# Optimization experiments

Hardware: AMD Instinct MI355X
Metric: run time of the kernel (lower is better)

The kernel has to match this reference:

```python
import jax, jax.numpy as jnp
import numpy as np

N, K, D, VOCAB = 20000, 32, 128, 100000
NEG = -1e30  # finite large-negative so all-masked rows don't produce NaN softmax


def setup_inputs() -> dict:
    key = jax.random.key(0)
    ks = jax.random.split(key, 10)
    return {
        "nodes": jax.random.randint(ks[0], (N,), 0, VOCAB),
        "neigh_idx": jax.random.randint(ks[1], (N, K), 0, VOCAB),
        "neigh_len": jax.random.randint(ks[2], (N,), 0, K + 1),
        "u2e": jax.random.normal(ks[3], (VOCAB, D), dtype=jnp.float32),
        "W1": jax.random.normal(ks[4], (D, 2 * D), dtype=jnp.float32) * 0.05,
        "b1": jax.random.normal(ks[5], (D,), dtype=jnp.float32) * 0.05,
        "W2": jax.random.normal(ks[6], (D, D), dtype=jnp.float32) * 0.05,
        "b2": jax.random.normal(ks[7], (D,), dtype=jnp.float32) * 0.05,
        "W3": jax.random.normal(ks[8], (1, D), dtype=jnp.float32) * 0.05,
        "b3": jax.random.normal(ks[9], (1,), dtype=jnp.float32) * 0.05,
    }


def reference(nodes, neigh_idx, neigh_len, u2e, W1, b1, W2, b2, W3, b3):
    # self features: [N, D]
    self_feats = u2e[nodes]
    # neighbor features gather: [N, K, D]
    e_u = u2e[neigh_idx]
    # GraphRec Attention: cat(neighbor, self-broadcast) -> MLP -> softmax over K
    x = jnp.concatenate(
        [e_u, jnp.broadcast_to(self_feats[:, None, :], e_u.shape)], axis=-1
    )  # [N, K, 2D]
    h = jax.nn.relu(jnp.einsum("nkf,df->nkd", x, W1) + b1)
    h = jax.nn.relu(jnp.einsum("nkd,ed->nke", h, W2) + b2)
    logits = jnp.einsum("nkd,od->nko", h, W3)[..., 0] + b3[0]  # [N, K]
    mask = jnp.arange(K)[None, :] < neigh_len[:, None]  # [N, K]
    att = jax.nn.softmax(jnp.where(mask, logits, NEG), axis=1)
    att = jnp.where(mask, att, 0.0)  # zero out padded slots (and all-empty rows)
    # attention-weighted neighbor aggregation: [N, D]
    agg = jnp.einsum("nk,nkd->nd", att, e_u)
    has_neigh = (neigh_len > 0)[:, None]
    return jnp.where(has_neigh, (agg + self_feats) * 0.5, self_feats)
```

## Files before the change

kernel.cpp:

```cpp
#include <hip/hip_runtime.h>
#include <hip/hip_bf16.h>
#include <stdint.h>

#define KN 32
#define D  128
#define NNODES 20000
#define GRID 2500
#define ITERS 4
#define VOCAB 100000
#define CONV_BLOCKS (VOCAB * D / 2048)

typedef __bf16 bf16;
typedef __bf16 bf16x8 __attribute__((ext_vector_type(8)));
typedef float  f32x4  __attribute__((ext_vector_type(4)));

#define CHUNK_E 520
#define EU_NODE_E (8 * CHUNK_E)
#define H_STRIDE 136

#define GL2LDS(src, dst) __builtin_amdgcn_global_load_lds(                 \
    (const __attribute__((address_space(1))) void*)(src),                  \
    (__attribute__((address_space(3))) void*)(dst), 16, 0, 0)

#define MFMA(a, b, c) __builtin_amdgcn_mfma_f32_16x16x32_bf16((a), (b), (c), 0, 0, 0)

#define LBAR() do {                                                        \
    asm volatile("s_waitcnt lgkmcnt(0)" ::: "memory");                     \
    __builtin_amdgcn_s_barrier();                                          \
    asm volatile("" ::: "memory");                                         \
    __builtin_amdgcn_sched_barrier(0);                                     \
} while (0)

__global__ __launch_bounds__(256) void pack_weights_kernel(
    const float* __restrict__ W1, const float* __restrict__ W2,
    bf16* __restrict__ w1p, bf16* __restrict__ w2p)
{
    int t = blockIdx.x * 256 + threadIdx.x;
    if (t < 32768) {
        int j = t & 7, lane = (t >> 3) & 63, kt = (t >> 9) & 7, nt = t >> 12;
        int d = nt * 16 + (lane & 15);
        int f = kt * 32 + ((lane >> 4) << 3) + j;
        w1p[t] = (bf16)W1[d * 256 + f];
    } else if (t < 49152) {
        int u = t - 32768;
        int j = u & 7, lane = (u >> 3) & 63, kt = (u >> 9) & 3, nt = u >> 11;
        int e  = nt * 16 + (lane & 15);
        int dd = kt * 32 + ((lane >> 4) << 3) + j;
        w2p[u] = (bf16)W2[e * 128 + dd];
    }
}

__global__ __launch_bounds__(256) void prep_kernel(
    const float* __restrict__ u2e, const float* __restrict__ W1,
    const float* __restrict__ W2,
    bf16* __restrict__ tbl, bf16* __restrict__ w1p, bf16* __restrict__ w2p)
{
    int b = blockIdx.x;
    if (b < CONV_BLOCKS) {
        size_t i = ((size_t)b * 256 + threadIdx.x) * 8;
        float4 a = *(const float4*)(u2e + i);
        float4 c = *(const float4*)(u2e + i + 4);
        bf16x8 v;
        v[0]=(bf16)a.x; v[1]=(bf16)a.y; v[2]=(bf16)a.z; v[3]=(bf16)a.w;
        v[4]=(bf16)c.x; v[5]=(bf16)c.y; v[6]=(bf16)c.z; v[7]=(bf16)c.w;
        *(bf16x8*)(tbl + i) = v;
    } else {
        int t = (b - CONV_BLOCKS) * 256 + threadIdx.x;
        if (t < 32768) {
            int j = t & 7, lane = (t >> 3) & 63, kt = (t >> 9) & 7, nt = t >> 12;
            int d = nt * 16 + (lane & 15);
            int f = kt * 32 + ((lane >> 4) << 3) + j;
            w1p[t] = (bf16)W1[d * 256 + f];
        } else if (t < 49152) {
            int u = t - 32768;
            int j = u & 7, lane = (u >> 3) & 63, kt = (u >> 9) & 3, nt = u >> 11;
            int e  = nt * 16 + (lane & 15);
            int dd = kt * 32 + ((lane >> 4) << 3) + j;
            w2p[u] = (bf16)W2[e * 128 + dd];
        }
    }
}

__global__ __launch_bounds__(256, 3) void graphrec_agg_kernel(
    const int*   __restrict__ nodes,
    const int*   __restrict__ neigh_idx,
    const int*   __restrict__ neigh_len,
    const float* __restrict__ u2e,
    const bf16*  __restrict__ u2e_bf,
    const float* __restrict__ b1,
    const float* __restrict__ b2,
    const float* __restrict__ W3,
    const float* __restrict__ b3,
    const bf16*  __restrict__ w1p,
    const bf16*  __restrict__ w2p,
    float*       __restrict__ out)
{
    __shared__ alignas(16) bf16  eu[2][2 * EU_NODE_E];
    __shared__ alignas(16) float self_f[2][2 * D];
    __shared__ alignas(16) bf16  h1[2 * KN * H_STRIDE];
    __shared__ float lpart[2][4 * KN];

    const int t    = threadIdx.x;
    const int lane = t & 63;
    const int wave = t >> 6;
    const int ln15 = lane & 15;
    const int quad = lane >> 4;
    const int nt0  = wave * 2;

    const float bias1_0 = b1[nt0 * 16 + ln15];
    const float bias1_1 = b1[(nt0 + 1) * 16 + ln15];
    const float bias2_0 = b2[nt0 * 16 + ln15];
    const float bias2_1 = b2[(nt0 + 1) * 16 + ln15];
    const float w3_0    = W3[nt0 * 16 + ln15];
    const float w3_1    = W3[(nt0 + 1) * 16 + ln15];
    const float b3v     = b3[0];

    bf16x8 w1e[2][4], w1s[2][4], w2r[2][4];
    #pragma unroll
    for (int nt = 0; nt < 2; ++nt) {
        #pragma unroll
        for (int ft = 0; ft < 4; ++ft) {
            w1e[nt][ft] = *(const bf16x8*)(w1p + ((nt0 + nt) * 8 + ft) * 512 + lane * 8);
            w1s[nt][ft] = *(const bf16x8*)(w1p + ((nt0 + nt) * 8 + 4 + ft) * 512 + lane * 8);
        }
        #pragma unroll
        for (int kt = 0; kt < 4; ++kt)
            w2r[nt][kt] = *(const bf16x8*)(w2p + ((nt0 + nt) * 4 + kt) * 512 + lane * 8);
    }

    auto STAGE = [&](int jt) {
        const int buf = jt & 1;
        const int nA2 = blockIdx.x * 8 + jt * 2;
        const int gnd = wave >> 1;
        const int cb  = (wave & 1) * 4;
        const int sA  = nodes[nA2];
        const int sB  = nodes[nA2 + 1];
        int4 idx4 = *(const int4*)(neigh_idx + (size_t)(nA2 + gnd) * KN + cb + (quad << 3));
        bf16* dst = &eu[buf][gnd * EU_NODE_E + cb * CHUNK_E];
        const size_t col = (size_t)(ln15 << 3);
        GL2LDS(u2e_bf + (size_t)idx4.x * D + col, dst);
        GL2LDS(u2e_bf + (size_t)idx4.y * D + col, dst + CHUNK_E);
        GL2LDS(u2e_bf + (size_t)idx4.z * D + col, dst + 2 * CHUNK_E);
        GL2LDS(u2e_bf + (size_t)idx4.w * D + col, dst + 3 * CHUNK_E);
        if (wave == 0) {
            int sidx = (lane >> 5) ? sB : sA;
            GL2LDS(u2e + (size_t)sidx * D + ((lane & 31) << 2), &self_f[buf][0]);
        }
    };

    STAGE(0);

    #pragma unroll 1
    for (int it = 0; it < ITERS; ++it) {
        const int nA   = blockIdx.x * 8 + it * 2;
        const int lenA = neigh_len[nA];
        const int lenB = neigh_len[nA + 1];

        if (it + 1 < ITERS) STAGE(it + 1);
        __builtin_amdgcn_sched_barrier(0);
        if (it == 0 || it + 1 == ITERS) {
            asm volatile("s_waitcnt vmcnt(0)" ::: "memory");
        } else if (wave == 0) {
            asm volatile("s_waitcnt vmcnt(6)" ::: "memory");
        } else {
            asm volatile("s_waitcnt vmcnt(5)" ::: "memory");
        }
        __builtin_amdgcn_s_barrier();
        asm volatile("" ::: "memory");
        __builtin_amdgcn_sched_barrier(0);

        const bf16*  euIt = &eu[it & 1][0];
        const float* sfIt = &self_f[it & 1][0];

        f32x4 cs0 = {0.f,0.f,0.f,0.f}, cs1 = cs0;
        {
            const float* sp = sfIt + (ln15 < 2 ? ln15 : 1) * D;
            #pragma unroll
            for (int kt = 0; kt < 4; ++kt) {
                f32x4 u0 = *(const f32x4*)(sp + kt * 32 + quad * 8);
                f32x4 u1 = *(const f32x4*)(sp + kt * 32 + quad * 8 + 4);
                bf16x8 a;
                #pragma unroll
                for (int e = 0; e < 4; ++e) { a[e] = (bf16)u0[e]; a[4 + e] = (bf16)u1[e]; }
                cs0 = MFMA(a, w1s[0][kt], cs0);
                cs1 = MFMA(a, w1s[1][kt], cs1);
            }
        }
        const float svA0 = __shfl(cs0[0], ln15);
        const float svB0 = __shfl(cs0[1], ln15);
        const float svA1 = __shfl(cs1[0], ln15);
        const float svB1 = __shfl(cs1[1], ln15);

        #pragma unroll 1
        for (int nd = 0; nd < 2; ++nd) {
            const bf16* euN = euIt + nd * EU_NODE_E;
            bf16* h1N = h1 + nd * KN * H_STRIDE;

            f32x4 c00 = {0.f,0.f,0.f,0.f}, c01 = c00, c10 = c00, c11 = c00;
            const int rb = (ln15 & 7) * CHUNK_E + (ln15 >> 3) * 128;
            #pragma unroll
            for (int ft = 0; ft < 4; ++ft) {
                bf16x8 a0 = *(const bf16x8*)(euN + rb + ft * 32 + quad * 8);
                bf16x8 a1 = *(const bf16x8*)(euN + rb + 256 + ft * 32 + quad * 8);
                c00 = MFMA(a0, w1e[0][ft], c00);
                c01 = MFMA(a0, w1e[1][ft], c01);
                c10 = MFMA(a1, w1e[0][ft], c10);
                c11 = MFMA(a1, w1e[1][ft], c11);
            }
            const float s0 = nd ? svB0 : svA0;
            const float s1 = nd ? svB1 : svA1;
            #pragma unroll
            for (int r = 0; r < 4; ++r) {
                int row = quad * 4 + r;
                h1N[row * H_STRIDE + nt0 * 16 + ln15]              = (bf16)fmaxf(c00[r] + bias1_0 + s0, 0.f);
                h1N[row * H_STRIDE + (nt0 + 1) * 16 + ln15]        = (bf16)fmaxf(c01[r] + bias1_1 + s1, 0.f);
                h1N[(16 + row) * H_STRIDE + nt0 * 16 + ln15]       = (bf16)fmaxf(c10[r] + bias1_0 + s0, 0.f);
                h1N[(16 + row) * H_STRIDE + (nt0 + 1) * 16 + ln15] = (bf16)fmaxf(c11[r] + bias1_1 + s1, 0.f);
            }
        }
        LBAR();

        #pragma unroll 1
        for (int nd = 0; nd < 2; ++nd) {
            const bf16* h1N = h1 + nd * KN * H_STRIDE;
            f32x4 d00 = {0.f,0.f,0.f,0.f}, d01 = d00, d10 = d00, d11 = d00;
            #pragma unroll
            for (int kt = 0; kt < 4; ++kt) {
                bf16x8 a0 = *(const bf16x8*)(h1N + ln15 * H_STRIDE + kt * 32 + quad * 8);
                bf16x8 a1 = *(const bf16x8*)(h1N + (16 + ln15) * H_STRIDE + kt * 32 + quad * 8);
                d00 = MFMA(a0, w2r[0][kt], d00);
                d01 = MFMA(a0, w2r[1][kt], d01);
                d10 = MFMA(a1, w2r[0][kt], d10);
                d11 = MFMA(a1, w2r[1][kt], d11);
            }
            #pragma unroll
            for (int r = 0; r < 4; ++r) {
                float p0 = w3_0 * fmaxf(d00[r] + bias2_0, 0.f)
                         + w3_1 * fmaxf(d01[r] + bias2_1, 0.f);
                float p1 = w3_0 * fmaxf(d10[r] + bias2_0, 0.f)
                         + w3_1 * fmaxf(d11[r] + bias2_1, 0.f);
                #pragma unroll
                for (int o = 1; o < 16; o <<= 1) {
                    p0 += __shfl_xor(p0, o);
                    p1 += __shfl_xor(p1, o);
                }
                if (ln15 == 0) {
                    lpart[nd][wave * KN + quad * 4 + r]      = p0;
                    lpart[nd][wave * KN + 16 + quad * 4 + r] = p1;
                }
            }
        }
        LBAR();

        {
            const int nd = wave >> 1;
            const int k  = lane & 31;
            float lg = lpart[nd][k] + lpart[nd][KN + k] + lpart[nd][2 * KN + k]
                     + lpart[nd][3 * KN + k] + b3v;
            const int len = nd ? lenB : lenA;
            bool act = k < len;
            float l = act ? lg : -1e30f;
            float m = l;
            #pragma unroll
            for (int o = 1; o < 32; o <<= 1) m = fmaxf(m, __shfl_xor(m, o));
            float e = act ? expf(l - m) : 0.f;
            float s = e;
            #pragma unroll
            for (int o = 1; o < 32; o <<= 1) s += __shfl_xor(s, o);
            float att = (s > 0.f) ? (e / s) : 0.f;

            const int d = ((wave & 1) << 6) + lane;
            const bf16* euN = euIt + nd * EU_NODE_E;
            float acc = 0.f;
            #pragma unroll
            for (int k2 = 0; k2 < KN; ++k2) {
                float a  = __shfl(att, k2);
                float ev = (float)euN[(k2 & 7) * CHUNK_E + (k2 >> 3) * 128 + (d & 127)];
                acc += a * ev;
            }
            float sf = sfIt[nd * D + (d & 127)];
            out[(size_t)(nA + nd) * D + (d & 127)] = (len > 0) ? 0.5f * (acc + sf) : sf;
        }
        LBAR();
    }
}

#define FB_CHUNK_DW 260
#define FB_EU_NODE_DW (16 * FB_CHUNK_DW)

__global__ __launch_bounds__(256, 3) void graphrec_agg_fb(
    const int*   __restrict__ nodes,
    const int*   __restrict__ neigh_idx,
    const int*   __restrict__ neigh_len,
    const float* __restrict__ u2e,
    const float* __restrict__ b1,
    const float* __restrict__ b2,
    const float* __restrict__ W3,
    const float* __restrict__ b3,
    const bf16*  __restrict__ w1p,
    const bf16*  __restrict__ w2p,
    float*       __restrict__ out)
{
    __shared__ alignas(16) float eu[2 * FB_EU_NODE_DW];
    __shared__ alignas(16) bf16  h1[2 * KN * H_STRIDE];
    __shared__ alignas(16) float self_f[2 * D];
    __shared__ float lpart[2][4 * KN];
    __shared__ float att_s[2][KN];

    const int t    = threadIdx.x;
    const int lane = t & 63;
    const int wave = t >> 6;
    const int ln15 = lane & 15;
    const int quad = lane >> 4;
    const int nt0  = wave * 2;

    const float bias1_0 = b1[nt0 * 16 + ln15];
    const float bias1_1 = b1[(nt0 + 1) * 16 + ln15];
    const float bias2_0 = b2[nt0 * 16 + ln15];
    const float bias2_1 = b2[(nt0 + 1) * 16 + ln15];
    const float w3_0    = W3[nt0 * 16 + ln15];
    const float w3_1    = W3[(nt0 + 1) * 16 + ln15];
    const float b3v     = b3[0];

    bf16x8 w1r[2][8];
    #pragma unroll
    for (int nt = 0; nt < 2; ++nt)
        #pragma unroll
        for (int ft = 0; ft < 8; ++ft)
            w1r[nt][ft] = *(const bf16x8*)(w1p + ((nt0 + nt) * 8 + ft) * 512 + lane * 8);
    bf16x8 w2r[2][4];
    #pragma unroll
    for (int nt = 0; nt < 2; ++nt)
        #pragma unroll
        for (int kt = 0; kt < 4; ++kt)
            w2r[nt][kt] = *(const bf16x8*)(w2p + ((nt0 + nt) * 4 + kt) * 512 + lane * 8);

    #pragma unroll 1
    for (int it = 0; it < ITERS; ++it) {
        const int nA   = blockIdx.x * 8 + it * 2;
        const int lenA = neigh_len[nA];
        const int lenB = neigh_len[nA + 1];
        {
            const int half = lane >> 5;
            const int colb = (lane & 31) << 4;
            #pragma unroll
            for (int nd = 0; nd < 2; ++nd) {
                #pragma unroll
                for (int j = 0; j < 4; ++j) {
                    int chunk = wave * 4 + j;
                    int idx = neigh_idx[(nA + nd) * KN + chunk + (half << 4)];
                    const char* src = (const char*)(u2e + (size_t)idx * D) + colb;
                    GL2LDS(src, eu + nd * FB_EU_NODE_DW + chunk * FB_CHUNK_DW);
                }
            }
            if (wave == 0) {
                int sidx = nodes[nA + half];
                const char* src = (const char*)(u2e + (size_t)sidx * D) + colb;
                GL2LDS(src, self_f);
            }
        }
        __syncthreads();
        #pragma unroll 1
        for (int nd = 0; nd < 2; ++nd) {
            const float* euN = eu + nd * FB_EU_NODE_DW;
            const float* sfN = self_f + nd * D;
            bf16* h1N = h1 + nd * KN * H_STRIDE;
            f32x4 c00 = {0.f,0.f,0.f,0.f}, c01 = c00, c10 = c00, c11 = c00;
            const int r0 = ln15 * FB_CHUNK_DW;
            #pragma unroll
            for (int ft = 0; ft < 4; ++ft) {
                int off = ft * 32 + quad * 8;
                f32x4 u0 = *(const f32x4*)(euN + r0 + off);
                f32x4 u1 = *(const f32x4*)(euN + r0 + off + 4);
                f32x4 v0 = *(const f32x4*)(euN + r0 + 128 + off);
                f32x4 v1 = *(const f32x4*)(euN + r0 + 128 + off + 4);
                bf16x8 a0, a1;
                #pragma unroll
                for (int e = 0; e < 4; ++e) {
                    a0[e] = (bf16)u0[e]; a0[4 + e] = (bf16)u1[e];
                    a1[e] = (bf16)v0[e]; a1[4 + e] = (bf16)v1[e];
                }
                c00 = MFMA(a0, w1r[0][ft], c00);
                c01 = MFMA(a0, w1r[1][ft], c01);
                c10 = MFMA(a1, w1r[0][ft], c10);
                c11 = MFMA(a1, w1r[1][ft], c11);
            }
            #pragma unroll
            for (int ft = 4; ft < 8; ++ft) {
                int off = (ft - 4) * 32 + quad * 8;
                f32x4 u0 = *(const f32x4*)(sfN + off);
                f32x4 u1 = *(const f32x4*)(sfN + off + 4);
                bf16x8 a;
                #pragma unroll
                for (int e = 0; e < 4; ++e) { a[e] = (bf16)u0[e]; a[4 + e] = (bf16)u1[e]; }
                c00 = MFMA(a, w1r[0][ft], c00);
                c01 = MFMA(a, w1r[1][ft], c01);
                c10 = MFMA(a, w1r[0][ft], c10);
                c11 = MFMA(a, w1r[1][ft], c11);
            }
            #pragma unroll
            for (int r = 0; r < 4; ++r) {
                int row = quad * 4 + r;
                h1N[row * H_STRIDE + nt0 * 16 + ln15]              = (bf16)fmaxf(c00[r] + bias1_0, 0.f);
                h1N[row * H_STRIDE + (nt0 + 1) * 16 + ln15]        = (bf16)fmaxf(c01[r] + bias1_1, 0.f);
                h1N[(16 + row) * H_STRIDE + nt0 * 16 + ln15]       = (bf16)fmaxf(c10[r] + bias1_0, 0.f);
                h1N[(16 + row) * H_STRIDE + (nt0 + 1) * 16 + ln15] = (bf16)fmaxf(c11[r] + bias1_1, 0.f);
            }
        }
        __syncthreads();
        #pragma unroll 1
        for (int nd = 0; nd < 2; ++nd) {
            const bf16* h1N = h1 + nd * KN * H_STRIDE;
            f32x4 d00 = {0.f,0.f,0.f,0.f}, d01 = d00, d10 = d00, d11 = d00;
            #pragma unroll
            for (int kt = 0; kt < 4; ++kt) {
                bf16x8 a0 = *(const bf16x8*)(h1N + ln15 * H_STRIDE + kt * 32 + quad * 8);
                bf16x8 a1 = *(const bf16x8*)(h1N + (16 + ln15) * H_STRIDE + kt * 32 + quad * 8);
                d00 = MFMA(a0, w2r[0][kt], d00);
                d01 = MFMA(a0, w2r[1][kt], d01);
                d10 = MFMA(a1, w2r[0][kt], d10);
                d11 = MFMA(a1, w2r[1][kt], d11);
            }
            #pragma unroll
            for (int r = 0; r < 4; ++r) {
                float p0 = w3_0 * fmaxf(d00[r] + bias2_0, 0.f)
                         + w3_1 * fmaxf(d01[r] + bias2_1, 0.f);
                float p1 = w3_0 * fmaxf(d10[r] + bias2_0, 0.f)
                         + w3_1 * fmaxf(d11[r] + bias2_1, 0.f);
                #pragma unroll
                for (int o = 1; o < 16; o <<= 1) {
                    p0 += __shfl_xor(p0, o);
                    p1 += __shfl_xor(p1, o);
                }
                if (ln15 == 0) {
                    lpart[nd][wave * KN + quad * 4 + r]      = p0;
                    lpart[nd][wave * KN + 16 + quad * 4 + r] = p1;
                }
            }
        }
        __syncthreads();
        if (wave < 2) {
            int nd = wave, k = lane & 31;
            float lg = lpart[nd][k] + lpart[nd][KN + k] + lpart[nd][2 * KN + k]
                     + lpart[nd][3 * KN + k] + b3v;
            int len = nd ? lenB : lenA;
            bool act = (lane < 32) && (k < len);
            float l = act ? lg : -1e30f;
            float m = l;
            #pragma unroll
            for (int o = 1; o < 32; o <<= 1) m = fmaxf(m, __shfl_xor(m, o));
            float e = act ? expf(l - m) : 0.f;
            float s = e;
            #pragma unroll
            for (int o = 1; o < 32; o <<= 1) s += __shfl_xor(s, o);
            if (lane < 32) att_s[nd][k] = (s > 0.f) ? (e / s) : 0.f;
        }
        __syncthreads();
        {
            int nd = t >> 7, d = t & 127;
            const float* euN = eu + nd * FB_EU_NODE_DW;
            float acc = 0.f;
            #pragma unroll
            for (int k = 0; k < KN; ++k)
                acc += att_s[nd][k] * euN[(k & 15) * FB_CHUNK_DW + ((k >> 4) << 7) + d];
            float sf = self_f[nd * D + d];
            int len = nd ? lenB : lenA;
            out[(size_t)(nA + nd) * D + d] = (len > 0) ? 0.5f * (acc + sf) : sf;
        }
        __syncthreads();
    }
}

extern "C" void kernel_launch(void* const* d_in, const int* in_sizes, int n_in,
                              void* d_out, int out_size, void* d_ws, size_t ws_size,
                              hipStream_t stream) {
    const int*   nodes     = (const int*)d_in[0];
    const int*   neigh_idx = (const int*)d_in[1];
    const int*   neigh_len = (const int*)d_in[2];
    const float* u2e       = (const float*)d_in[3];
    const float* W1        = (const float*)d_in[4];
    const float* b1        = (const float*)d_in[5];
    const float* W2        = (const float*)d_in[6];
    const float* b2        = (const float*)d_in[7];
    const float* W3        = (const float*)d_in[8];
    const float* b3        = (const float*)d_in[9];
    float* out = (float*)d_out;

    bf16*  w1p    = (bf16*)d_ws;
    bf16*  w2p    = w1p + 32768;
    bf16*  u2e_bf = (bf16*)((char*)d_ws + 98304);
    const size_t need = 98304ull + (size_t)VOCAB * D * 2;

    if (ws_size >= need) {
        prep_kernel<<<CONV_BLOCKS + 192, 256, 0, stream>>>(u2e, W1, W2,
                                                           u2e_bf, w1p, w2p);
        graphrec_agg_kernel<<<GRID, 256, 0, stream>>>(nodes, neigh_idx, neigh_len,
                                                      u2e, u2e_bf, b1, b2,
                                                      W3, b3, w1p, w2p, out);
    } else {
        pack_weights_kernel<<<192, 256, 0, stream>>>(W1, W2, w1p, w2p);
        graphrec_agg_fb<<<GRID, 256, 0, stream>>>(nodes, neigh_idx, neigh_len, u2e,
                                                  b1, b2, W3, b3, w1p, w2p, out);
    }
}
```

Measured before the change: 212.9 us.

## Process one node per iteration and precompute self projections up front

Each loop iteration of the main kernel now handles one node instead of two, with eight iterations per block, so the eu, h1 and lpart shared buffers shrink by half. The self-feature half of the first MLP layer is computed once before the loop for all eight nodes, using bf16 table rows and a single MFMA batch. This removes the per-iteration self MFMAs and frees the w1s registers. The launch bound goes from 3 to 4 blocks per CU to raise occupancy, but each iteration does less work between barriers, so barrier and latency overhead per node rises, and half the lanes sit idle in the final store.

```diff
diff --git a/kernel.cpp b/kernel.cpp
--- a/kernel.cpp
+++ b/kernel.cpp
@@ -6,7 +6,7 @@
 #define D  128
 #define NNODES 20000
 #define GRID 2500
-#define ITERS 4
+#define ITERS 8
 #define VOCAB 100000
 #define CONV_BLOCKS (VOCAB * D / 2048)
 
@@ -81,7 +81,7 @@
     }
 }
 
-__global__ __launch_bounds__(256, 3) void graphrec_agg_kernel(
+__global__ __launch_bounds__(256, 4) void graphrec_agg_kernel(
     const int*   __restrict__ nodes,
     const int*   __restrict__ neigh_idx,
     const int*   __restrict__ neigh_len,
@@ -95,10 +95,10 @@
     const bf16*  __restrict__ w2p,
     float*       __restrict__ out)
 {
-    __shared__ alignas(16) bf16  eu[2][2 * EU_NODE_E];
-    __shared__ alignas(16) float self_f[2][2 * D];
-    __shared__ alignas(16) bf16  h1[2 * KN * H_STRIDE];
-    __shared__ float lpart[2][4 * KN];
+    __shared__ alignas(16) bf16  eu[2][EU_NODE_E];
+    __shared__ alignas(16) bf16  h1[KN * H_STRIDE];
+    __shared__ float lpart[4 * KN];
+    __shared__ alignas(16) float self_s[2][256];
 
     const int t    = threadIdx.x;
     const int lane = t & 63;
@@ -106,6 +106,7 @@
     const int ln15 = lane & 15;
     const int quad = lane >> 4;
     const int nt0  = wave * 2;
+    const int r0   = blockIdx.x * ITERS;
 
     const float bias1_0 = b1[nt0 * 16 + ln15];
     const float bias1_1 = b1[(nt0 + 1) * 16 + ln15];
@@ -115,87 +116,63 @@
     const float w3_1    = W3[(nt0 + 1) * 16 + ln15];
     const float b3v     = b3[0];
 
-    bf16x8 w1e[2][4], w1s[2][4], w2r[2][4];
+    f32x4 cs0 = {0.f,0.f,0.f,0.f}, cs1 = cs0;
+    {
+        int nid = nodes[r0 + (ln15 & 7)];
+        #pragma unroll
+        for (int kt = 0; kt < 4; ++kt) {
+            bf16x8 a  = *(const bf16x8*)(u2e_bf + (size_t)nid * D + kt * 32 + quad * 8);
+            bf16x8 b0 = *(const bf16x8*)(w1p + (nt0 * 8 + 4 + kt) * 512 + lane * 8);
+            bf16x8 b1f= *(const bf16x8*)(w1p + ((nt0 + 1) * 8 + 4 + kt) * 512 + lane * 8);
+            cs0 = MFMA(a, b0, cs0);
+            cs1 = MFMA(a, b1f, cs1);
+        }
+    }
+
+    bf16x8 w1e[2][4], w2r[2][4];
     #pragma unroll
     for (int nt = 0; nt < 2; ++nt) {
         #pragma unroll
-        for (int ft = 0; ft < 4; ++ft) {
+        for (int ft = 0; ft < 4; ++ft)
             w1e[nt][ft] = *(const bf16x8*)(w1p + ((nt0 + nt) * 8 + ft) * 512 + lane * 8);
-            w1s[nt][ft] = *(const bf16x8*)(w1p + ((nt0 + nt) * 8 + 4 + ft) * 512 + lane * 8);
-        }
         #pragma unroll
         for (int kt = 0; kt < 4; ++kt)
             w2r[nt][kt] = *(const bf16x8*)(w2p + ((nt0 + nt) * 4 + kt) * 512 + lane * 8);
     }
 
     auto STAGE = [&](int jt) {
-        const int buf = jt & 1;
-        const int nA2 = blockIdx.x * 8 + jt * 2;
-        const int gnd = wave >> 1;
-        const int cb  = (wave & 1) * 4;
-        const int sA  = nodes[nA2];
-        const int sB  = nodes[nA2 + 1];
-        int4 idx4 = *(const int4*)(neigh_idx + (size_t)(nA2 + gnd) * KN + cb + (quad << 3));
-        bf16* dst = &eu[buf][gnd * EU_NODE_E + cb * CHUNK_E];
+        const int slot = jt & 1;
+        const int n    = r0 + jt;
+        const int c0   = wave * 2;
+        int2 idx2 = *(const int2*)(neigh_idx + (size_t)n * KN + c0 + (quad << 3));
+        bf16* dst = &eu[slot][c0 * CHUNK_E];
         const size_t col = (size_t)(ln15 << 3);
-        GL2LDS(u2e_bf + (size_t)idx4.x * D + col, dst);
-        GL2LDS(u2e_bf + (size_t)idx4.y * D + col, dst + CHUNK_E);
-        GL2LDS(u2e_bf + (size_t)idx4.z * D + col, dst + 2 * CHUNK_E);
-        GL2LDS(u2e_bf + (size_t)idx4.w * D + col, dst + 3 * CHUNK_E);
-        if (wave == 0) {
-            int sidx = (lane >> 5) ? sB : sA;
-            GL2LDS(u2e + (size_t)sidx * D + ((lane & 31) << 2), &self_f[buf][0]);
-        }
+        GL2LDS(u2e_bf + (size_t)idx2.x * D + col, dst);
+        GL2LDS(u2e_bf + (size_t)idx2.y * D + col, dst + CHUNK_E);
+        int sidx = nodes[n];
+        GL2LDS(u2e + (size_t)sidx * D + ((size_t)(lane & 31) << 2), &self_s[slot][0]);
     };
 
     STAGE(0);
 
     #pragma unroll 1
     for (int it = 0; it < ITERS; ++it) {
-        const int nA   = blockIdx.x * 8 + it * 2;
-        const int lenA = neigh_len[nA];
-        const int lenB = neigh_len[nA + 1];
-
+        const int n = r0 + it;
+
+        __builtin_amdgcn_sched_barrier(0);
         if (it + 1 < ITERS) STAGE(it + 1);
         __builtin_amdgcn_sched_barrier(0);
-        if (it == 0 || it + 1 == ITERS) {
-            asm volatile("s_waitcnt vmcnt(0)" ::: "memory");
-        } else if (wave == 0) {
-            asm volatile("s_waitcnt vmcnt(6)" ::: "memory");
-        } else {
-            asm volatile("s_waitcnt vmcnt(5)" ::: "memory");
-        }
+        if (it == 0)                 asm volatile("s_waitcnt vmcnt(4)" ::: "memory");
+        else if (it + 1 == ITERS)    asm volatile("s_waitcnt vmcnt(1)" ::: "memory");
+        else                         asm volatile("s_waitcnt vmcnt(5)" ::: "memory");
         __builtin_amdgcn_s_barrier();
         asm volatile("" ::: "memory");
         __builtin_amdgcn_sched_barrier(0);
 
-        const bf16*  euIt = &eu[it & 1][0];
-        const float* sfIt = &self_f[it & 1][0];
-
-        f32x4 cs0 = {0.f,0.f,0.f,0.f}, cs1 = cs0;
+        const int len = neigh_len[n];
+        const bf16* euN = &eu[it & 1][0];
+
         {
-            const float* sp = sfIt + (ln15 < 2 ? ln15 : 1) * D;
-            #pragma unroll
-            for (int kt = 0; kt < 4; ++kt) {
-                f32x4 u0 = *(const f32x4*)(sp + kt * 32 + quad * 8);
-                f32x4 u1 = *(const f32x4*)(sp + kt * 32 + quad * 8 + 4);
-                bf16x8 a;
-                #pragma unroll
-                for (int e = 0; e < 4; ++e) { a[e] = (bf16)u0[e]; a[4 + e] = (bf16)u1[e]; }
-                cs0 = MFMA(a, w1s[0][kt], cs0);
-                cs1 = MFMA(a, w1s[1][kt], cs1);
-            }
-        }
-        const float svA0 = __shfl(cs0[0], ln15);
-        const float svB0 = __shfl(cs0[1], ln15);
-        const float svA1 = __shfl(cs1[0], ln15);
-        const float svB1 = __shfl(cs1[1], ln15);
-
-        #pragma unroll 1
-        for (int nd = 0; nd < 2; ++nd) {
-            const bf16* euN = euIt + nd * EU_NODE_E;
-            bf16* h1N = h1 + nd * KN * H_STRIDE;
-
             f32x4 c00 = {0.f,0.f,0.f,0.f}, c01 = c00, c10 = c00, c11 = c00;
             const int rb = (ln15 & 7) * CHUNK_E + (ln15 >> 3) * 128;
             #pragma unroll
@@ -207,27 +184,30 @@
                 c10 = MFMA(a1, w1e[0][ft], c10);
                 c11 = MFMA(a1, w1e[1][ft], c11);
             }
-            const float s0 = nd ? svB0 : svA0;
-            const float s1 = nd ? svB1 : svA1;
+            float sel0 = (it & 2) ? ((it & 1) ? cs0[3] : cs0[2])
+                                  : ((it & 1) ? cs0[1] : cs0[0]);
+            float sel1 = (it & 2) ? ((it & 1) ? cs1[3] : cs1[2])
+                                  : ((it & 1) ? cs1[1] : cs1[0]);
+            const int srcl = ((it >> 2) << 4) + ln15;
+            const float s0 = __shfl(sel0, srcl);
+            const float s1 = __shfl(sel1, srcl);
             #pragma unroll
             for (int r = 0; r < 4; ++r) {
                 int row = quad * 4 + r;
-                h1N[row * H_STRIDE + nt0 * 16 + ln15]              = (bf16)fmaxf(c00[r] + bias1_0 + s0, 0.f);
-                h1N[row * H_STRIDE + (nt0 + 1) * 16 + ln15]        = (bf16)fmaxf(c01[r] + bias1_1 + s1, 0.f);
-                h1N[(16 + row) * H_STRIDE + nt0 * 16 + ln15]       = (bf16)fmaxf(c10[r] + bias1_0 + s0, 0.f);
-                h1N[(16 + row) * H_STRIDE + (nt0 + 1) * 16 + ln15] = (bf16)fmaxf(c11[r] + bias1_1 + s1, 0.f);
+                h1[row * H_STRIDE + nt0 * 16 + ln15]              = (bf16)fmaxf(c00[r] + bias1_0 + s0, 0.f);
+                h1[row * H_STRIDE + (nt0 + 1) * 16 + ln15]        = (bf16)fmaxf(c01[r] + bias1_1 + s1, 0.f);
+                h1[(16 + row) * H_STRIDE + nt0 * 16 + ln15]       = (bf16)fmaxf(c10[r] + bias1_0 + s0, 0.f);
+                h1[(16 + row) * H_STRIDE + (nt0 + 1) * 16 + ln15] = (bf16)fmaxf(c11[r] + bias1_1 + s1, 0.f);
             }
         }
         LBAR();
 
-        #pragma unroll 1
-        for (int nd = 0; nd < 2; ++nd) {
-            const bf16* h1N = h1 + nd * KN * H_STRIDE;
+        {
             f32x4 d00 = {0.f,0.f,0.f,0.f}, d01 = d00, d10 = d00, d11 = d00;
             #pragma unroll
             for (int kt = 0; kt < 4; ++kt) {
-                bf16x8 a0 = *(const bf16x8*)(h1N + ln15 * H_STRIDE + kt * 32 + quad * 8);
-                bf16x8 a1 = *(const bf16x8*)(h1N + (16 + ln15) * H_STRIDE + kt * 32 + quad * 8);
+                bf16x8 a0 = *(const bf16x8*)(h1 + ln15 * H_STRIDE + kt * 32 + quad * 8);
+                bf16x8 a1 = *(const bf16x8*)(h1 + (16 + ln15) * H_STRIDE + kt * 32 + quad * 8);
                 d00 = MFMA(a0, w2r[0][kt], d00);
                 d01 = MFMA(a0, w2r[1][kt], d01);
                 d10 = MFMA(a1, w2r[0][kt], d10);
@@ -245,19 +225,17 @@
                     p1 += __shfl_xor(p1, o);
                 }
                 if (ln15 == 0) {
-                    lpart[nd][wave * KN + quad * 4 + r]      = p0;
-                    lpart[nd][wave * KN + 16 + quad * 4 + r] = p1;
+                    lpart[wave * KN + quad * 4 + r]      = p0;
+                    lpart[wave * KN + 16 + quad * 4 + r] = p1;
                 }
             }
         }
         LBAR();
 
         {
-            const int nd = wave >> 1;
-            const int k  = lane & 31;
-            float lg = lpart[nd][k] + lpart[nd][KN + k] + lpart[nd][2 * KN + k]
-                     + lpart[nd][3 * KN + k] + b3v;
-            const int len = nd ? lenB : lenA;
+            const int k = lane & 31;
+            float lg = lpart[k] + lpart[KN + k] + lpart[2 * KN + k]
+                     + lpart[3 * KN + k] + b3v;
             bool act = k < len;
             float l = act ? lg : -1e30f;
             float m = l;
@@ -269,17 +247,17 @@
             for (int o = 1; o < 32; o <<= 1) s += __shfl_xor(s, o);
             float att = (s > 0.f) ? (e / s) : 0.f;
 
-            const int d = ((wave & 1) << 6) + lane;
-            const bf16* euN = euIt + nd * EU_NODE_E;
+            const int cw = wave * 32 + k;
             float acc = 0.f;
             #pragma unroll
             for (int k2 = 0; k2 < KN; ++k2) {
                 float a  = __shfl(att, k2);
-                float ev = (float)euN[(k2 & 7) * CHUNK_E + (k2 >> 3) * 128 + (d & 127)];
+                float ev = (float)euN[(k2 & 7) * CHUNK_E + (k2 >> 3) * 128 + cw];
                 acc += a * ev;
             }
-            float sf = sfIt[nd * D + (d & 127)];
-            out[(size_t)(nA + nd) * D + (d & 127)] = (len > 0) ? 0.5f * (acc + sf) : sf;
+            float sf = self_s[it & 1][cw];
+            if (lane < 32)
+                out[(size_t)n * D + cw] = (len > 0) ? 0.5f * (acc + sf) : sf;
         }
         LBAR();
     }
@@ -287,6 +265,7 @@
 
 #define FB_CHUNK_DW 260
 #define FB_EU_NODE_DW (16 * FB_CHUNK_DW)
+#define FB_ITERS 4
 
 __global__ __launch_bounds__(256, 3) void graphrec_agg_fb(
     const int*   __restrict__ nodes,
@@ -336,7 +315,7 @@
             w2r[nt][kt] = *(const bf16x8*)(w2p + ((nt0 + nt) * 4 + kt) * 512 + lane * 8);
 
     #pragma unroll 1
-    for (int it = 0; it < ITERS; ++it) {
+    for (int it = 0; it < FB_ITERS; ++it) {
         const int nA   = blockIdx.x * 8 + it * 2;
         const int lenA = neigh_len[nA];
         const int lenB = neigh_len[nA + 1];
```

New measurement: 254.9 us. 19.8% more time.

## Drop double-buffered prefetch for higher occupancy and hoist self projection

Applied to the files above, without the earlier changes.

Removes the double-buffered LDS staging of neighbor and self features so each iteration loads and then synchronizes, halving shared memory for those buffers. Launch bounds are raised to four blocks per CU, relying on cross-block parallelism to hide gather latency instead of in-block prefetch. The self-feature half of the first layer is computed once per block for all eight nodes via MFMA from the bf16 table and selected per iteration with shuffles. This risks exposing load latency within each block and may raise register pressure under the tighter occupancy target.

```diff
diff --git a/kernel.cpp b/kernel.cpp
--- a/kernel.cpp
+++ b/kernel.cpp
@@ -23,13 +23,6 @@
     (__attribute__((address_space(3))) void*)(dst), 16, 0, 0)
 
 #define MFMA(a, b, c) __builtin_amdgcn_mfma_f32_16x16x32_bf16((a), (b), (c), 0, 0, 0)
-
-#define LBAR() do {                                                        \
-    asm volatile("s_waitcnt lgkmcnt(0)" ::: "memory");                     \
-    __builtin_amdgcn_s_barrier();                                          \
-    asm volatile("" ::: "memory");                                         \
-    __builtin_amdgcn_sched_barrier(0);                                     \
-} while (0)
 
 __global__ __launch_bounds__(256) void pack_weights_kernel(
     const float* __restrict__ W1, const float* __restrict__ W2,
@@ -81,7 +74,7 @@
     }
 }
 
-__global__ __launch_bounds__(256, 3) void graphrec_agg_kernel(
+__global__ __launch_bounds__(256, 4) void graphrec_agg_kernel(
     const int*   __restrict__ nodes,
     const int*   __restrict__ neigh_idx,
     const int*   __restrict__ neigh_len,
@@ -95,8 +88,8 @@
     const bf16*  __restrict__ w2p,
     float*       __restrict__ out)
 {
-    __shared__ alignas(16) bf16  eu[2][2 * EU_NODE_E];
-    __shared__ alignas(16) float self_f[2][2 * D];
+    __shared__ alignas(16) bf16  eu[2 * EU_NODE_E];
+    __shared__ alignas(16) float self_f[2 * D];
     __shared__ alignas(16) bf16  h1[2 * KN * H_STRIDE];
     __shared__ float lpart[2][4 * KN];
 
@@ -115,40 +108,31 @@
     const float w3_1    = W3[(nt0 + 1) * 16 + ln15];
     const float b3v     = b3[0];
 
-    bf16x8 w1e[2][4], w1s[2][4], w2r[2][4];
+    f32x4 cs0 = {0.f,0.f,0.f,0.f}, cs1 = cs0;
+    {
+        int nid = nodes[blockIdx.x * 8 + (ln15 & 7)];
+        #pragma unroll
+        for (int kt = 0; kt < 4; ++kt) {
+            bf16x8 a   = *(const bf16x8*)(u2e_bf + (size_t)nid * D + kt * 32 + quad * 8);
+            bf16x8 bb0 = *(const bf16x8*)(w1p + (nt0 * 8 + 4 + kt) * 512 + lane * 8);
+            bf16x8 bb1 = *(const bf16x8*)(w1p + ((nt0 + 1) * 8 + 4 + kt) * 512 + lane * 8);
+            cs0 = MFMA(a, bb0, cs0);
+            cs1 = MFMA(a, bb1, cs1);
+        }
+    }
+
+    bf16x8 w1r[2][4];
     #pragma unroll
-    for (int nt = 0; nt < 2; ++nt) {
+    for (int nt = 0; nt < 2; ++nt)
         #pragma unroll
-        for (int ft = 0; ft < 4; ++ft) {
-            w1e[nt][ft] = *(const bf16x8*)(w1p + ((nt0 + nt) * 8 + ft) * 512 + lane * 8);
-            w1s[nt][ft] = *(const bf16x8*)(w1p + ((nt0 + nt) * 8 + 4 + ft) * 512 + lane * 8);
-        }
+        for (int ft = 0; ft < 4; ++ft)
+            w1r[nt][ft] = *(const bf16x8*)(w1p + ((nt0 + nt) * 8 + ft) * 512 + lane * 8);
+    bf16x8 w2r[2][4];
+    #pragma unroll
+    for (int nt = 0; nt < 2; ++nt)
         #pragma unroll
         for (int kt = 0; kt < 4; ++kt)
             w2r[nt][kt] = *(const bf16x8*)(w2p + ((nt0 + nt) * 4 + kt) * 512 + lane * 8);
-    }
-
-    auto STAGE = [&](int jt) {
-        const int buf = jt & 1;
-        const int nA2 = blockIdx.x * 8 + jt * 2;
-        const int gnd = wave >> 1;
-        const int cb  = (wave & 1) * 4;
-        const int sA  = nodes[nA2];
-        const int sB  = nodes[nA2 + 1];
-        int4 idx4 = *(const int4*)(neigh_idx + (size_t)(nA2 + gnd) * KN + cb + (quad << 3));
-        bf16* dst = &eu[buf][gnd * EU_NODE_E + cb * CHUNK_E];
-        const size_t col = (size_t)(ln15 << 3);
-        GL2LDS(u2e_bf + (size_t)idx4.x * D + col, dst);
-        GL2LDS(u2e_bf + (size_t)idx4.y * D + col, dst + CHUNK_E);
-        GL2LDS(u2e_bf + (size_t)idx4.z * D + col, dst + 2 * CHUNK_E);
-        GL2LDS(u2e_bf + (size_t)idx4.w * D + col, dst + 3 * CHUNK_E);
-        if (wave == 0) {
-            int sidx = (lane >> 5) ? sB : sA;
-            GL2LDS(u2e + (size_t)sidx * D + ((lane & 31) << 2), &self_f[buf][0]);
-        }
-    };
-
-    STAGE(0);
 
     #pragma unroll 1
     for (int it = 0; it < ITERS; ++it) {
@@ -156,44 +140,37 @@
         const int lenA = neigh_len[nA];
         const int lenB = neigh_len[nA + 1];
 
-        if (it + 1 < ITERS) STAGE(it + 1);
-        __builtin_amdgcn_sched_barrier(0);
-        if (it == 0 || it + 1 == ITERS) {
-            asm volatile("s_waitcnt vmcnt(0)" ::: "memory");
-        } else if (wave == 0) {
-            asm volatile("s_waitcnt vmcnt(6)" ::: "memory");
-        } else {
-            asm volatile("s_waitcnt vmcnt(5)" ::: "memory");
-        }
-        __builtin_amdgcn_s_barrier();
-        asm volatile("" ::: "memory");
-        __builtin_amdgcn_sched_barrier(0);
-
-        const bf16*  euIt = &eu[it & 1][0];
-        const float* sfIt = &self_f[it & 1][0];
-
-        f32x4 cs0 = {0.f,0.f,0.f,0.f}, cs1 = cs0;
         {
-            const float* sp = sfIt + (ln15 < 2 ? ln15 : 1) * D;
-            #pragma unroll
-            for (int kt = 0; kt < 4; ++kt) {
-                f32x4 u0 = *(const f32x4*)(sp + kt * 32 + quad * 8);
-                f32x4 u1 = *(const f32x4*)(sp + kt * 32 + quad * 8 + 4);
-                bf16x8 a;
-                #pragma unroll
-                for (int e = 0; e < 4; ++e) { a[e] = (bf16)u0[e]; a[4 + e] = (bf16)u1[e]; }
-                cs0 = MFMA(a, w1s[0][kt], cs0);
-                cs1 = MFMA(a, w1s[1][kt], cs1);
-            }
-        }
-        const float svA0 = __shfl(cs0[0], ln15);
-        const float svB0 = __shfl(cs0[1], ln15);
-        const float svA1 = __shfl(cs1[0], ln15);
-        const float svB1 = __shfl(cs1[1], ln15);
+            const int gnd = wave >> 1;
+            const int cb  = (wave & 1) * 4;
+            #pragma unroll
+            for (int j = 0; j < 4; ++j) {
+                int chunk = cb + j;
+                int idx = neigh_idx[(nA + gnd) * KN + chunk + ((lane >> 4) << 3)];
+                GL2LDS(u2e_bf + (size_t)idx * D + ((lane & 15) << 3),
+                       eu + gnd * EU_NODE_E + chunk * CHUNK_E);
+            }
+            if (wave == 0) {
+                int sidx = nodes[nA + (lane >> 5)];
+                GL2LDS(u2e + (size_t)sidx * D + ((lane & 31) << 2), self_f);
+            }
+        }
+        __syncthreads();
+
+        const bool hi = (it & 1);
+        const float selA0 = hi ? cs0[2] : cs0[0];
+        const float selB0 = hi ? cs0[3] : cs0[1];
+        const float selA1 = hi ? cs1[2] : cs1[0];
+        const float selB1 = hi ? cs1[3] : cs1[1];
+        const int   srcl  = ((it >> 1) << 4) + ln15;
+        const float svA0 = __shfl(selA0, srcl);
+        const float svB0 = __shfl(selB0, srcl);
+        const float svA1 = __shfl(selA1, srcl);
+        const float svB1 = __shfl(selB1, srcl);
 
         #pragma unroll 1
         for (int nd = 0; nd < 2; ++nd) {
-            const bf16* euN = euIt + nd * EU_NODE_E;
+            const bf16* euN = eu + nd * EU_NODE_E;
             bf16* h1N = h1 + nd * KN * H_STRIDE;
 
             f32x4 c00 = {0.f,0.f,0.f,0.f}, c01 = c00, c10 = c00, c11 = c00;
@@ -202,10 +179,10 @@
             for (int ft = 0; ft < 4; ++ft) {
                 bf16x8 a0 = *(const bf16x8*)(euN + rb + ft * 32 + quad * 8);
                 bf16x8 a1 = *(const bf16x8*)(euN + rb + 256 + ft * 32 + quad * 8);
-                c00 = MFMA(a0, w1e[0][ft], c00);
-                c01 = MFMA(a0, w1e[1][ft], c01);
-                c10 = MFMA(a1, w1e[0][ft], c10);
-                c11 = MFMA(a1, w1e[1][ft], c11);
+                c00 = MFMA(a0, w1r[0][ft], c00);
+                c01 = MFMA(a0, w1r[1][ft], c01);
+                c10 = MFMA(a1, w1r[0][ft], c10);
+                c11 = MFMA(a1, w1r[1][ft], c11);
             }
             const float s0 = nd ? svB0 : svA0;
             const float s1 = nd ? svB1 : svA1;
@@ -218,7 +195,7 @@
                 h1N[(16 + row) * H_STRIDE + (nt0 + 1) * 16 + ln15] = (bf16)fmaxf(c11[r] + bias1_1 + s1, 0.f);
             }
         }
-        LBAR();
+        __syncthreads();
 
         #pragma unroll 1
         for (int nd = 0; nd < 2; ++nd) {
@@ -250,7 +227,7 @@
                 }
             }
         }
-        LBAR();
+        __syncthreads();
 
         {
             const int nd = wave >> 1;
@@ -270,7 +247,7 @@
             float att = (s > 0.f) ? (e / s) : 0.f;
 
             const int d = ((wave & 1) << 6) + lane;
-            const bf16* euN = euIt + nd * EU_NODE_E;
+            const bf16* euN = eu + nd * EU_NODE_E;
             float acc = 0.f;
             #pragma unroll
             for (int k2 = 0; k2 < KN; ++k2) {
@@ -278,10 +255,10 @@
                 float ev = (float)euN[(k2 & 7) * CHUNK_E + (k2 >> 3) * 128 + (d & 127)];
                 acc += a * ev;
             }
-            float sf = sfIt[nd * D + (d & 127)];
+            float sf = self_f[nd * D + (d & 127)];
             out[(size_t)(nA + nd) * D + (d & 127)] = (len > 0) ? 0.5f * (acc + sf) : sf;
         }
-        LBAR();
+        __syncthreads();
     }
 }
 
@@ -336,7 +313,7 @@
             w2r[nt][kt] = *(const bf16x8*)(w2p + ((nt0 + nt) * 4 + kt) * 512 + lane * 8);
 
     #pragma unroll 1
-    for (int it = 0; it < ITERS; ++it) {
+    for (int it = 0; it < 4; ++it) {
         const int nA   = blockIdx.x * 8 + it * 2;
         const int lenA = neigh_len[nA];
         const int lenB = neigh_len[nA + 1];
```

After: 216.1 us. About the same (+1.5%).
